# Kernel tuning notes

Hardware: AMD Instinct MI355X
Metric: run time of the kernel (lower is better)

## Reference

```python
import jax, jax.numpy as jnp
import numpy as np

N, E, F_NODE, F_EDGE, H, EH, G = 20000, 200000, 32, 8, 256, 16, 512
OUT_DIMS = [H, H, H // 2]  # 256, 256, 128
BN_EPS = 1e-5


def _lin(k, out_c, in_c):
    kw, kb = jax.random.split(k)
    bound = 1.0 / np.sqrt(in_c)
    w = jax.random.uniform(kw, (out_c, in_c), minval=-bound, maxval=bound, dtype=jnp.float32)
    b = jax.random.uniform(kb, (out_c,), minval=-bound, maxval=bound, dtype=jnp.float32)
    return w, b


def setup_inputs() -> dict:
    key = jax.random.key(0)
    ks = jax.random.split(key, 40)
    inp = {
        "x": jax.random.normal(ks[0], (N, F_NODE), dtype=jnp.float32),
        "edge_index": jax.random.randint(ks[1], (2, E), 0, N, dtype=jnp.int64),
        "edge_attr": jax.random.normal(ks[2], (E, F_EDGE), dtype=jnp.float32),
        "batch": jnp.sort(jax.random.randint(ks[3], (N,), 0, G, dtype=jnp.int64)),
    }
    inp["ee_w"], inp["ee_b"] = _lin(ks[4], EH, F_EDGE)
    inp["ne_w"], inp["ne_b"] = _lin(ks[5], H, F_NODE)
    in_dim = H
    for i, out_dim in enumerate(OUT_DIMS):
        msg_in = 2 * in_dim + EH
        inp[f"c{i}_w1"], inp[f"c{i}_b1"] = _lin(ks[6 + 2 * i], 2 * out_dim, msg_in)
        inp[f"c{i}_w2"], inp[f"c{i}_b2"] = _lin(ks[7 + 2 * i], out_dim, 2 * out_dim)
        inp[f"bn{i}_g"] = jnp.ones((out_dim,), jnp.float32)
        inp[f"bn{i}_b"] = jnp.zeros((out_dim,), jnp.float32)
        inp[f"bn{i}_m"] = jnp.zeros((out_dim,), jnp.float32)
        inp[f"bn{i}_v"] = jnp.ones((out_dim,), jnp.float32)
        in_dim = out_dim
    inp["fc_w"], inp["fc_b"] = _lin(ks[20], 12, H // 2)
    return inp


def _seg_mean(vals, idx, num):
    s = jax.ops.segment_sum(vals, idx, num_segments=num)
    cnt = jax.ops.segment_sum(jnp.ones((vals.shape[0],), vals.dtype), idx, num_segments=num)
    return s / jnp.maximum(cnt, 1.0)[:, None]


def reference(x, edge_index, edge_attr, batch,
              ee_w, ee_b, ne_w, ne_b,
              c0_w1, c0_b1, c0_w2, c0_b2,
              c1_w1, c1_b1, c1_w2, c1_b2,
              c2_w1, c2_b1, c2_w2, c2_b2,
              bn0_g, bn0_b, bn0_m, bn0_v,
              bn1_g, bn1_b, bn1_m, bn1_v,
              bn2_g, bn2_b, bn2_m, bn2_v,
              fc_w, fc_b):
    src, dst = edge_index[0], edge_index[1]  # x_j = source, x_i = target
    e = jax.nn.relu(edge_attr @ ee_w.T + ee_b)  # [E, EH]
    h = jax.nn.relu(x @ ne_w.T + ne_b)          # [N, H]
    convs = [(c0_w1, c0_b1, c0_w2, c0_b2), (c1_w1, c1_b1, c1_w2, c1_b2), (c2_w1, c2_b1, c2_w2, c2_b2)]
    bns = [(bn0_g, bn0_b, bn0_m, bn0_v), (bn1_g, bn1_b, bn1_m, bn1_v), (bn2_g, bn2_b, bn2_m, bn2_v)]
    for (w1, b1, w2, b2), (g, bb, rm, rv) in zip(convs, bns):
        m = jnp.concatenate([h[dst], h[src], e], axis=1)      # [E, 2*in + EH]
        m = jax.nn.relu(m @ w1.T + b1) @ w2.T + b2            # per-edge MLP
        h = _seg_mean(m, dst, N)                              # scatter-mean to targets
        h = jax.nn.relu((h - rm) / jnp.sqrt(rv + BN_EPS) * g + bb)  # eval-mode BN
        # dropout is identity in eval mode
    pooled = _seg_mean(h, batch, G)                           # global_mean_pool [G, H//2]
    return jax.nn.sigmoid(pooled @ fc_w.T + fc_b)             # [G, 12]
```

## Files before the change

kernel.cpp:

```cpp
#include <hip/hip_runtime.h>
#include <hip/hip_bf16.h>

typedef unsigned int  uint;
typedef unsigned short ushort;
typedef float  f32x2  __attribute__((ext_vector_type(2)));
typedef float  f32x4  __attribute__((ext_vector_type(4)));
typedef __bf16 bf16x8 __attribute__((ext_vector_type(8)));

#define DEV static __device__ __forceinline__

DEV float  b2f(ushort b){ return __uint_as_float(((uint)b) << 16); }
DEV float  lo2f(uint u){ return __uint_as_float(u << 16); }
DEV float  hi2f(uint u){ return __uint_as_float(u & 0xffff0000u); }
DEV ushort f2b(float f){
  uint u = __float_as_uint(f);
  u += 0x7fffu + ((u >> 16) & 1u);
  return (ushort)(u >> 16);
}
DEV uint pk2(float a, float b){ return (uint)f2b(a) | ((uint)f2b(b) << 16); }
DEV void unpack8(uint4 v, float* f){
  f[0]=lo2f(v.x); f[1]=hi2f(v.x); f[2]=lo2f(v.y); f[3]=hi2f(v.y);
  f[4]=lo2f(v.z); f[5]=hi2f(v.z); f[6]=lo2f(v.w); f[7]=hi2f(v.w);
}
DEV int ld_idx(const void* p, int flag, long long i){
  return flag ? ((const int*)p)[i] : (int)((const long long*)p)[i];
}
DEV int clampi(int v, int lo, int hi){ return v < lo ? lo : (v > hi ? hi : v); }

DEV void ld16(const ushort* g, ushort* l){
  __builtin_amdgcn_global_load_lds(
      (const __attribute__((address_space(1))) void*)g,
      (__attribute__((address_space(3))) void*)l, 16, 0, 0);
}

__global__ void k_probes(const uint* __restrict__ ei, const uint* __restrict__ xw,
                         int* __restrict__ iflag, int* __restrict__ fflag){
  __shared__ int anyI, cntF;
  if (threadIdx.x == 0){ anyI = 0; cntF = 0; }
  __syncthreads();
  int li = 0, lc = 0;
  for (int i = threadIdx.x; i < 1024; i += 256){
    if (ei[2*i + 1] != 0u) li = 1;
    float f = fabsf(__uint_as_float(xw[i]));
    if (f > 1e-6f && f < 1e6f) lc++;
  }
  if (li) atomicOr(&anyI, 1);
  atomicAdd(&cntF, lc);
  __syncthreads();
  if (threadIdx.x == 0){ *iflag = anyI; *fflag = (2*cntF > 1024) ? 1 : 0; }
}

__global__ __launch_bounds__(256) void k_canon(const void* __restrict__ src,
    const int* __restrict__ flag, int* __restrict__ out, int n){
  int i = blockIdx.x*256 + threadIdx.x;
  if (i >= n) return;
  out[i] = ld_idx(src, *flag, i);
}

struct CvtTab { const void* src[8]; ushort* dst[8]; int n[8]; int bstart[8]; int nseg; };
__global__ __launch_bounds__(256) void k_cvt_batch(CvtTab tab, const int* __restrict__ flag){
  int b = blockIdx.x;
  int s = tab.nseg - 1;
  for (int i = 1; i < tab.nseg; i++) if (b < tab.bstart[i]){ s = i - 1; break; }
  int rel = b - tab.bstart[s];
  const void* sp = tab.src[s];
  ushort* d = tab.dst[s];
  int f = *flag;
  int end = tab.n[s]; int cap = rel*8192 + 8192; if (cap < end) end = cap;
  for (int i = rel*8192 + threadIdx.x; i < end; i += 256)
    d[i] = f ? f2b(((const float*)sp)[i]) : ((const ushort*)sp)[i];
}

struct SmallTab { const void* src[24]; int doff[24]; int n[24]; };
__global__ __launch_bounds__(256) void k_cvt_small(SmallTab tab, const int* __restrict__ flag,
    ushort* __restrict__ base, int cnt){
  int b = blockIdx.x;
  if (b >= cnt) return;
  int f = *flag;
  const void* s = tab.src[b];
  ushort* d = base + tab.doff[b];
  for (int i = threadIdx.x; i < tab.n[b]; i += 256)
    d[i] = f ? f2b(((const float*)s)[i]) : ((const ushort*)s)[i];
}

__global__ __launch_bounds__(256) void k_count(const void* __restrict__ ei,
    const int* __restrict__ flag, int* __restrict__ cnt, int E, int N){
  int e = blockIdx.x*256 + threadIdx.x;
  if (e >= E) return;
  int d = clampi(ld_idx(ei, *flag, (long long)E + e), 0, N-1);
  atomicAdd(&cnt[d], 1);
}

__global__ __launch_bounds__(1024) void k_scan(const int* __restrict__ deg, int* __restrict__ rp, int n){
  __shared__ int part[1024];
  int t = threadIdx.x;
  int chunk = (n + 1023) >> 10;
  int base = t * chunk;
  int s = 0;
  for (int i = 0; i < chunk; i++){ int j = base + i; if (j < n) s += deg[j]; }
  part[t] = s;
  __syncthreads();
  for (int off = 1; off < 1024; off <<= 1){
    int v = (t >= off) ? part[t - off] : 0;
    __syncthreads();
    part[t] += v;
    __syncthreads();
  }
  int run = part[t] - s;
  for (int i = 0; i < chunk; i++){ int j = base + i; if (j < n){ rp[j] = run; run += deg[j]; } }
  if (t == 1023) rp[n] = part[1023];
}

__global__ __launch_bounds__(256) void k_fill(const void* __restrict__ ei,
    const int* __restrict__ flag, const int* __restrict__ rp, int* __restrict__ fill,
    int2* __restrict__ cpair, int E, int N){
  int e = blockIdx.x*256 + threadIdx.x;
  if (e >= E) return;
  int f = *flag;
  int s = clampi(ld_idx(ei, f, e), 0, N-1);
  int d = clampi(ld_idx(ei, f, (long long)E + e), 0, N-1);
  int pos = clampi(rp[d] + atomicAdd(&fill[d], 1), 0, E-1);
  cpair[pos] = make_int2(s, e);
}

__global__ __launch_bounds__(256) void k_edge_enc(const void* __restrict__ ea,
    const ushort* __restrict__ w, const ushort* __restrict__ b,
    const int* __restrict__ fflag, float* __restrict__ eh, int E){
  __shared__ float ws[128];
  __shared__ float bs[16];
  int t = threadIdx.x;
  if (t < 128) ws[t] = b2f(w[t]);
  if (t < 16)  bs[t] = b2f(b[t]);
  int f = *fflag;
  __syncthreads();
  int e = blockIdx.x*256 + t;
  if (e >= E) return;
  float a[8];
  if (f){
    const float4* ap = (const float4*)((const float*)ea + (size_t)e*8);
    float4 v0 = ap[0], v1 = ap[1];
    a[0]=v0.x; a[1]=v0.y; a[2]=v0.z; a[3]=v0.w;
    a[4]=v1.x; a[5]=v1.y; a[6]=v1.z; a[7]=v1.w;
  } else {
    uint4 av = *(const uint4*)((const ushort*)ea + (size_t)e*8);
    unpack8(av, a);
  }
  float o[16];
  #pragma unroll
  for (int c = 0; c < 16; c++){
    float s = bs[c];
    #pragma unroll
    for (int j = 0; j < 8; j++) s += a[j]*ws[c*8+j];
    o[c] = fmaxf(s, 0.f);
  }
  f32x4* op = (f32x4*)(eh + (size_t)e*16);
  #pragma unroll
  for (int q4 = 0; q4 < 4; q4++){
    f32x4 v = {o[q4*4+0], o[q4*4+1], o[q4*4+2], o[q4*4+3]};
    op[q4] = v;
  }
}

__global__ __launch_bounds__(256) void k_node_enc(const void* __restrict__ x,
    const ushort* __restrict__ w, const ushort* __restrict__ b,
    const int* __restrict__ fflag, ushort* __restrict__ h, int N){
  __shared__ float xs[4][32];
  int nb = blockIdx.x*4, t = threadIdx.x;
  int f = *fflag;
  if (t < 128){
    int ni = t >> 5, ci = t & 31;
    int n = nb + ni; if (n >= N) n = N - 1;
    xs[ni][ci] = f ? ((const float*)x)[(size_t)n*32 + ci]
                   : b2f(((const ushort*)x)[(size_t)n*32 + ci]);
  }
  __syncthreads();
  const uint4* wp = (const uint4*)(w + (size_t)t*32);
  float wr[32];
  unpack8(wp[0], wr); unpack8(wp[1], wr+8); unpack8(wp[2], wr+16); unpack8(wp[3], wr+24);
  float bv = b2f(b[t]);
  #pragma unroll
  for (int ni = 0; ni < 4; ni++){
    int n = nb + ni;
    if (n >= N) break;
    float s = bv;
    #pragma unroll
    for (int k = 0; k < 32; k++) s += xs[ni][k]*wr[k];
    h[(size_t)n*256 + t] = f2b(fmaxf(s, 0.f));
  }
}

__global__ __launch_bounds__(256) void k_gemm_pq_lds(const ushort* __restrict__ A,
    const ushort* __restrict__ w1, int M, int Nc,
    ushort* __restrict__ P, ushort* __restrict__ Q){
  __shared__ ushort As[128*32];
  __shared__ ushort Bs[128*32];
  const int t = threadIdx.x;
  const int lane = t & 63;
  const int wv = t >> 6;
  const int m0 = blockIdx.x*128;
  const int yc = Nc >> 7;
  const int isQ = (int)blockIdx.y >= yc;
  const int n0 = (isQ ? blockIdx.y - yc : blockIdx.y)*128;
  const ushort* W = w1 + (isQ ? 256 : 0);
  ushort* C = isQ ? Q : P;
  const int lr = lane & 15;
  const int qq = lane >> 4;
  int srow0 = t >> 2,         sq0 = t & 3;
  int srow1 = (256 + t) >> 2, sq1 = t & 3;
  int ga0 = m0 + srow0; if (ga0 >= M) ga0 = M - 1;
  int ga1 = m0 + srow1; if (ga1 >= M) ga1 = M - 1;
  f32x4 acc[2][8];
  #pragma unroll
  for (int f = 0; f < 2; f++)
    #pragma unroll
    for (int j = 0; j < 8; j++) acc[f][j] = {0.f,0.f,0.f,0.f};
  for (int k0 = 0; k0 < 256; k0 += 32){
    ld16(A + (size_t)ga0*256 + k0 + sq0*8, &As[(size_t)t*8]);
    ld16(A + (size_t)ga1*256 + k0 + sq1*8, &As[(size_t)(256+t)*8]);
    ld16(W + (size_t)(n0 + srow0)*528 + k0 + sq0*8, &Bs[(size_t)t*8]);
    ld16(W + (size_t)(n0 + srow1)*528 + k0 + sq1*8, &Bs[(size_t)(256+t)*8]);
    __syncthreads();
    bf16x8 a0 = *(const bf16x8*)&As[(wv*32 + lr)*32 + qq*8];
    bf16x8 a1 = *(const bf16x8*)&As[(wv*32 + 16 + lr)*32 + qq*8];
    #pragma unroll
    for (int j = 0; j < 8; j++){
      bf16x8 b = *(const bf16x8*)&Bs[(j*16 + lr)*32 + qq*8];
      acc[0][j] = __builtin_amdgcn_mfma_f32_16x16x32_bf16(a0, b, acc[0][j], 0, 0, 0);
      acc[1][j] = __builtin_amdgcn_mfma_f32_16x16x32_bf16(a1, b, acc[1][j], 0, 0, 0);
    }
    __syncthreads();
  }
  #pragma unroll
  for (int f = 0; f < 2; f++){
    #pragma unroll
    for (int r = 0; r < 4; r++){
      int row = m0 + wv*32 + f*16 + qq*4 + r;
      if (row >= M) continue;
      #pragma unroll
      for (int j = 0; j < 8; j++)
        C[(size_t)row*Nc + n0 + j*16 + lr] = f2b(acc[f][j][r]);
    }
  }
}

__global__ __launch_bounds__(256) void k_gemm_bn64(const ushort* __restrict__ A, int lda,
    const ushort* __restrict__ W, int ldb, int M, int Nc, int K,
    const ushort* __restrict__ bias, const ushort* __restrict__ g, const ushort* __restrict__ bb,
    const ushort* __restrict__ rm, const ushort* __restrict__ rv,
    const int* __restrict__ rp, ushort* __restrict__ H){
  __shared__ ushort As[64*32];
  __shared__ ushort Bs[128*32];
  const int t = threadIdx.x;
  const int lane = t & 63;
  const int wv = t >> 6;
  const int m0 = blockIdx.x*64;
  const int n0 = blockIdx.y*128;
  const int lr = lane & 15;
  const int qq = lane >> 4;
  int srowA = t >> 2, sqA = t & 3;
  int ga = m0 + srowA; if (ga >= M) ga = M - 1;
  int srowB0 = t >> 2,        srowB1 = 64 + (t >> 2);
  f32x4 acc[8];
  #pragma unroll
  for (int j = 0; j < 8; j++) acc[j] = {0.f,0.f,0.f,0.f};
  for (int k0 = 0; k0 < K; k0 += 32){
    ld16(A + (size_t)ga*lda + k0 + sqA*8, &As[(size_t)t*8]);
    ld16(W + (size_t)(n0 + srowB0)*ldb + k0 + sqA*8, &Bs[(size_t)t*8]);
    ld16(W + (size_t)(n0 + srowB1)*ldb + k0 + sqA*8, &Bs[(size_t)(256+t)*8]);
    __syncthreads();
    bf16x8 a = *(const bf16x8*)&As[(wv*16 + lr)*32 + qq*8];
    #pragma unroll
    for (int j = 0; j < 8; j++){
      bf16x8 b = *(const bf16x8*)&Bs[(j*16 + lr)*32 + qq*8];
      acc[j] = __builtin_amdgcn_mfma_f32_16x16x32_bf16(a, b, acc[j], 0, 0, 0);
    }
    __syncthreads();
  }
  float bi[8], sc[8], sh[8];
  #pragma unroll
  for (int j = 0; j < 8; j++){
    int col = n0 + j*16 + lr;
    bi[j] = b2f(bias[col]);
    sc[j] = b2f(g[col]) * rsqrtf(b2f(rv[col]) + 1e-5f);
    sh[j] = b2f(bb[col]) - b2f(rm[col]) * sc[j];
  }
  #pragma unroll
  for (int r = 0; r < 4; r++){
    int row = m0 + wv*16 + qq*4 + r;
    if (row >= M) continue;
    int empty = (rp[row+1] - rp[row] == 0);
    #pragma unroll
    for (int j = 0; j < 8; j++){
      float v = acc[j][r] + bi[j];
      if (empty) v = 0.f;
      H[(size_t)row*Nc + n0 + j*16 + lr] = f2b(fmaxf(v*sc[j] + sh[j], 0.f));
    }
  }
}

template<int C>
__global__ __launch_bounds__(256) void k_msg4(const ushort* P, const ushort* __restrict__ Q,
    const float* __restrict__ eh, const ushort* __restrict__ w1, const ushort* __restrict__ b1,
    const int* __restrict__ rp, const int2* __restrict__ cpair,
    ushort* MU, int N){
  int t = threadIdx.x;
  int c0 = t*2;
  f32x2 wc[16];
  {
    float a0[16], a1[16];
    const uint4* wp0 = (const uint4*)(w1 + (size_t)c0*528 + 512);
    const uint4* wp1 = (const uint4*)(w1 + (size_t)(c0+1)*528 + 512);
    unpack8(wp0[0], a0); unpack8(wp0[1], a0+8);
    unpack8(wp1[0], a1); unpack8(wp1[1], a1+8);
    #pragma unroll
    for (int j = 0; j < 16; j++){ wc[j].x = a0[j]; wc[j].y = a1[j]; }
  }
  uint bw = *(const uint*)(b1 + c0);
  f32x2 b1v = { lo2f(bw), hi2f(bw) };
  int nb = blockIdx.x*2;
  int ne = nb + 2; if (ne > N) ne = N;
  for (int n = nb; n < ne; n++){
    const int i0 = rp[n], i1 = rp[n+1];
    uint pw = *(const uint*)(P + (size_t)n*C + c0);
    f32x2 pre = { lo2f(pw) + b1v.x, hi2f(pw) + b1v.y };
    f32x2 acc0 = {0.f, 0.f}, acc1 = {0.f, 0.f};
    int i = i0;
    for (; i + 2 <= i1; i += 2){
      int2 p0 = cpair[i];
      int2 p1 = cpair[i+1];
      uint qw0 = *(const uint*)(Q + (size_t)p0.x*C + c0);
      uint qw1 = *(const uint*)(Q + (size_t)p1.x*C + c0);
      const f32x4* e0p = (const f32x4*)(eh + (size_t)p0.y*16);
      const f32x4* e1p = (const f32x4*)(eh + (size_t)p1.y*16);
      f32x4 ea0 = e0p[0], ea1 = e0p[1], ea2 = e0p[2], ea3 = e0p[3];
      f32x4 eb0 = e1p[0], eb1 = e1p[1], eb2 = e1p[2], eb3 = e1p[3];
      float ef0[16] = {ea0.x,ea0.y,ea0.z,ea0.w, ea1.x,ea1.y,ea1.z,ea1.w,
                       ea2.x,ea2.y,ea2.z,ea2.w, ea3.x,ea3.y,ea3.z,ea3.w};
      float ef1[16] = {eb0.x,eb0.y,eb0.z,eb0.w, eb1.x,eb1.y,eb1.z,eb1.w,
                       eb2.x,eb2.y,eb2.z,eb2.w, eb3.x,eb3.y,eb3.z,eb3.w};
      f32x2 d0 = { pre.x + lo2f(qw0), pre.y + hi2f(qw0) };
      f32x2 d1 = { pre.x + lo2f(qw1), pre.y + hi2f(qw1) };
      #pragma unroll
      for (int j = 0; j < 16; j++){
        f32x2 e0v = {ef0[j], ef0[j]};
        f32x2 e1v = {ef1[j], ef1[j]};
        d0 += wc[j] * e0v;
        d1 += wc[j] * e1v;
      }
      acc0.x += fmaxf(d0.x, 0.f); acc0.y += fmaxf(d0.y, 0.f);
      acc1.x += fmaxf(d1.x, 0.f); acc1.y += fmaxf(d1.y, 0.f);
    }
    if (i < i1){
      int2 p0 = cpair[i];
      uint qw0 = *(const uint*)(Q + (size_t)p0.x*C + c0);
      const f32x4* e0p = (const f32x4*)(eh + (size_t)p0.y*16);
      f32x4 ea0 = e0p[0], ea1 = e0p[1], ea2 = e0p[2], ea3 = e0p[3];
      float ef0[16] = {ea0.x,ea0.y,ea0.z,ea0.w, ea1.x,ea1.y,ea1.z,ea1.w,
                       ea2.x,ea2.y,ea2.z,ea2.w, ea3.x,ea3.y,ea3.z,ea3.w};
      f32x2 d0 = { pre.x + lo2f(qw0), pre.y + hi2f(qw0) };
      #pragma unroll
      for (int j = 0; j < 16; j++){
        f32x2 e0v = {ef0[j], ef0[j]};
        d0 += wc[j] * e0v;
      }
      acc0.x += fmaxf(d0.x, 0.f); acc0.y += fmaxf(d0.y, 0.f);
    }
    int cnt = i1 - i0;
    float inv = (cnt > 0) ? 1.f/(float)cnt : 0.f;
    *(uint*)(MU + (size_t)n*C + c0) = pk2((acc0.x + acc1.x)*inv, (acc0.y + acc1.y)*inv);
  }
}

__global__ __launch_bounds__(128) void k_pool(const ushort* __restrict__ h, const int* __restrict__ batch,
    const ushort* __restrict__ fw, const ushort* __restrict__ fb,
    const int* __restrict__ fflag, void* __restrict__ out, int N){
  int g = blockIdx.x, t = threadIdx.x;
  int lo = 0, hi = N;
  while (lo < hi){ int mid = (lo+hi) >> 1; if (batch[mid] <  g) lo = mid+1; else hi = mid; }
  int s0 = lo;
  hi = N;
  while (lo < hi){ int mid = (lo+hi) >> 1; if (batch[mid] <= g) lo = mid+1; else hi = mid; }
  int s1 = lo;
  float s = 0.f;
  for (int i = s0; i < s1; i++) s += b2f(h[(size_t)i*128 + t]);
  int cnt = s1 - s0;
  __shared__ float ps[128];
  ps[t] = s / (float)(cnt > 0 ? cnt : 1);
  __syncthreads();
  if (t < 12){
    float z = b2f(fb[t]);
    for (int j = 0; j < 128; j++) z += ps[j]*b2f(fw[t*128 + j]);
    float r = 1.f/(1.f + expf(-z));
    if (*fflag) ((float*)out)[g*12 + t] = r;
    else        ((ushort*)out)[g*12 + t] = f2b(r);
  }
}

__global__ __launch_bounds__(256) void k_sentinel(ushort* __restrict__ out, int n){
  int i = blockIdx.x*256 + threadIdx.x;
  if (i < n) out[i] = 0x3F00;
}

extern "C" void kernel_launch(void* const* d_in, const int* in_sizes, int n_in,
                              void* d_out, int out_size, void* d_ws, size_t ws_size,
                              hipStream_t stream){
  const void* x_raw   = d_in[0];
  const void* ei_raw  = d_in[1];
  const void* ea_raw  = d_in[2];
  const void* ba_raw  = d_in[3];
  (void)n_in;

  const int N = in_sizes[3];
  const int E = in_sizes[1] / 2;
  const int G = out_size / 12;

  char* base = (char*)d_ws;
  size_t off = 0;
  auto alloc = [&](size_t bytes)->char*{
    char* p = base + off;
    off = (off + bytes + 255) & ~(size_t)255;
    return p;
  };
  int* iflag    = (int*)alloc(256);
  int* fflag    = (int*)alloc(256);
  int* deg      = (int*)alloc((size_t)N*4);
  int* fill     = (int*)alloc((size_t)N*4);
  size_t memset_bytes = (size_t)((char*)fill - (char*)deg) + (size_t)N*4;
  int* rp       = (int*)alloc((size_t)(N+1)*4);
  int* batch2   = (int*)alloc((size_t)N*4);
  int2* cpair   = (int2*)alloc((size_t)E*8);
  ushort* new_c = (ushort*)alloc(8192*2);
  ushort* w1c[3], *w2c[3];
  const int w1n[3] = {512*528, 512*528, 256*528};
  const int w2n[3] = {256*512, 256*512, 128*256};
  for (int i = 0; i < 3; i++) w1c[i] = (ushort*)alloc((size_t)w1n[i]*2);
  for (int i = 0; i < 3; i++) w2c[i] = (ushort*)alloc((size_t)w2n[i]*2);
  ushort* smallp = (ushort*)alloc(8192*2);
  float*  e_h32 = (float*)alloc((size_t)E*16*4);
  ushort* h     = (ushort*)alloc((size_t)N*256*2);
  ushort* Q     = (ushort*)alloc((size_t)N*512*2);
  ushort* PM    = (ushort*)alloc((size_t)N*512*2);

  if (off > ws_size){
    k_sentinel<<<(out_size + 255)/256, 256, 0, stream>>>((ushort*)d_out, out_size);
    return;
  }

  k_probes<<<1, 256, 0, stream>>>((const uint*)ei_raw, (const uint*)x_raw, iflag, fflag);
  k_canon<<<(N + 255)/256, 256, 0, stream>>>(ba_raw, iflag, batch2, N);
  hipMemsetAsync(deg, 0, memset_bytes, stream);
  k_count<<<(E + 255)/256, 256, 0, stream>>>(ei_raw, iflag, deg, E, N);
  k_scan<<<1, 1024, 0, stream>>>(deg, rp, N);
  k_fill<<<(E + 255)/256, 256, 0, stream>>>(ei_raw, iflag, rp, fill, cpair, E, N);

  CvtTab ct; ct.nseg = 7;
  const void* csrcs[7] = {d_in[8], d_in[16], d_in[24], d_in[10], d_in[18], d_in[26], d_in[6]};
  ushort* cdsts[7]     = {w1c[0],  w1c[1],   w1c[2],   w2c[0],   w2c[1],   w2c[2],   new_c};
  const int cns[7]     = {w1n[0],  w1n[1],   w1n[2],   w2n[0],   w2n[1],   w2n[2],   8192};
  int bacc = 0;
  for (int i = 0; i < 7; i++){
    ct.src[i] = csrcs[i]; ct.dst[i] = cdsts[i]; ct.n[i] = cns[i];
    ct.bstart[i] = bacc; bacc += (cns[i] + 8191)/8192;
  }
  k_cvt_batch<<<bacc, 256, 0, stream>>>(ct, fflag);

  SmallTab tab;
  int scount = 0, spos = 0;
  auto addsmall = [&](int di, int n)->int{
    int p = spos;
    tab.src[scount] = d_in[di]; tab.doff[scount] = spos; tab.n[scount] = n;
    spos += n; scount++;
    return p;
  };
  int pos_eew  = addsmall(4, 128);
  int pos_eeb  = addsmall(5, 16);
  int pos_neb  = addsmall(7, 256);
  int pos_b1[3], pos_b2[3], pos_g[3], pos_bb[3], pos_m[3], pos_v[3];
  const int b1n[3] = {512,512,256}, b2n[3] = {256,256,128}, bnn[3] = {256,256,128};
  for (int i = 0; i < 3; i++){
    int di = 8 + 8*i;
    pos_b1[i] = addsmall(di+1, b1n[i]);
    pos_b2[i] = addsmall(di+3, b2n[i]);
    pos_g[i]  = addsmall(di+4, bnn[i]);
    pos_bb[i] = addsmall(di+5, bnn[i]);
    pos_m[i]  = addsmall(di+6, bnn[i]);
    pos_v[i]  = addsmall(di+7, bnn[i]);
  }
  int pos_fcw = addsmall(32, 12*128);
  int pos_fcb = addsmall(33, 12);
  k_cvt_small<<<scount, 256, 0, stream>>>(tab, fflag, smallp, scount);

  k_edge_enc<<<(E + 255)/256, 256, 0, stream>>>(ea_raw, smallp + pos_eew, smallp + pos_eeb, fflag, e_h32, E);
  k_node_enc<<<(N + 3)/4, 256, 0, stream>>>(x_raw, new_c, smallp + pos_neb, fflag, h, N);

  const int Cch[3] = {512, 512, 256};
  const int Od[3]  = {256, 256, 128};
  for (int i = 0; i < 3; i++){
    dim3 g1((N + 127)/128, 2*(Cch[i]/128));
    k_gemm_pq_lds<<<g1, 256, 0, stream>>>(h, w1c[i], N, Cch[i], PM, Q);
    dim3 gm((N + 1)/2);
    if (i < 2) k_msg4<512><<<gm, 256, 0, stream>>>(PM, Q, e_h32, w1c[i], smallp + pos_b1[i], rp, cpair, PM, N);
    else       k_msg4<256><<<gm, 128, 0, stream>>>(PM, Q, e_h32, w1c[i], smallp + pos_b1[i], rp, cpair, PM, N);
    dim3 g2((N + 63)/64, Od[i]/128 > 0 ? Od[i]/128 : 1);
    k_gemm_bn64<<<g2, 256, 0, stream>>>(PM, Cch[i], w2c[i], Cch[i], N, Od[i], Cch[i],
                                        smallp + pos_b2[i], smallp + pos_g[i], smallp + pos_bb[i],
                                        smallp + pos_m[i],  smallp + pos_v[i], rp, h);
  }

  k_pool<<<G, 128, 0, stream>>>(h, batch2, smallp + pos_fcw, smallp + pos_fcb, fflag, d_out, N);
}
```

Before: 516.2 us.

## Merge preprocessing kernels into one mega-kernel and read small params directly

Folds the flag probe and the zeroing of counters into one kernel, replacing the memset. The CSR fill, weight conversion, edge encoder and node encoder are merged into a single block-partitioned launch. The small-parameter conversion and batch canonicalisation kernels are dropped; biases, BN params, the pool weights and the batch index are now read from the raw inputs with a runtime dtype flag. This cuts launch count and serial dependencies at the cost of per-element branching on the flag.

```diff
diff --git a/kernel.cpp b/kernel.cpp
--- a/kernel.cpp
+++ b/kernel.cpp
@@ -25,6 +25,9 @@
 DEV int ld_idx(const void* p, int flag, long long i){
   return flag ? ((const int*)p)[i] : (int)((const long long*)p)[i];
 }
+DEV float ldf(const void* p, int f, int i){
+  return f ? ((const float*)p)[i] : b2f(((const ushort*)p)[i]);
+}
 DEV int clampi(int v, int lo, int hi){ return v < lo ? lo : (v > hi ? hi : v); }
 
 DEV void ld16(const ushort* g, ushort* l){
@@ -33,54 +36,26 @@
       (__attribute__((address_space(3))) void*)l, 16, 0, 0);
 }
 
-__global__ void k_probes(const uint* __restrict__ ei, const uint* __restrict__ xw,
-                         int* __restrict__ iflag, int* __restrict__ fflag){
-  __shared__ int anyI, cntF;
-  if (threadIdx.x == 0){ anyI = 0; cntF = 0; }
-  __syncthreads();
-  int li = 0, lc = 0;
-  for (int i = threadIdx.x; i < 1024; i += 256){
-    if (ei[2*i + 1] != 0u) li = 1;
-    float f = fabsf(__uint_as_float(xw[i]));
-    if (f > 1e-6f && f < 1e6f) lc++;
-  }
-  if (li) atomicOr(&anyI, 1);
-  atomicAdd(&cntF, lc);
-  __syncthreads();
-  if (threadIdx.x == 0){ *iflag = anyI; *fflag = (2*cntF > 1024) ? 1 : 0; }
-}
-
-__global__ __launch_bounds__(256) void k_canon(const void* __restrict__ src,
-    const int* __restrict__ flag, int* __restrict__ out, int n){
+__global__ __launch_bounds__(256) void k_zero_probe(const uint* __restrict__ ei,
+    const uint* __restrict__ xw, int* __restrict__ iflag, int* __restrict__ fflag,
+    int* __restrict__ zbase, int zn){
   int i = blockIdx.x*256 + threadIdx.x;
-  if (i >= n) return;
-  out[i] = ld_idx(src, *flag, i);
-}
-
-struct CvtTab { const void* src[8]; ushort* dst[8]; int n[8]; int bstart[8]; int nseg; };
-__global__ __launch_bounds__(256) void k_cvt_batch(CvtTab tab, const int* __restrict__ flag){
-  int b = blockIdx.x;
-  int s = tab.nseg - 1;
-  for (int i = 1; i < tab.nseg; i++) if (b < tab.bstart[i]){ s = i - 1; break; }
-  int rel = b - tab.bstart[s];
-  const void* sp = tab.src[s];
-  ushort* d = tab.dst[s];
-  int f = *flag;
-  int end = tab.n[s]; int cap = rel*8192 + 8192; if (cap < end) end = cap;
-  for (int i = rel*8192 + threadIdx.x; i < end; i += 256)
-    d[i] = f ? f2b(((const float*)sp)[i]) : ((const ushort*)sp)[i];
-}
-
-struct SmallTab { const void* src[24]; int doff[24]; int n[24]; };
-__global__ __launch_bounds__(256) void k_cvt_small(SmallTab tab, const int* __restrict__ flag,
-    ushort* __restrict__ base, int cnt){
-  int b = blockIdx.x;
-  if (b >= cnt) return;
-  int f = *flag;
-  const void* s = tab.src[b];
-  ushort* d = base + tab.doff[b];
-  for (int i = threadIdx.x; i < tab.n[b]; i += 256)
-    d[i] = f ? f2b(((const float*)s)[i]) : ((const ushort*)s)[i];
+  if (i < zn) zbase[i] = 0;
+  if (blockIdx.x == 0){
+    __shared__ int anyI, cntF;
+    if (threadIdx.x == 0){ anyI = 0; cntF = 0; }
+    __syncthreads();
+    int li = 0, lc = 0;
+    for (int k = threadIdx.x; k < 1024; k += 256){
+      if (ei[2*k + 1] != 0u) li = 1;
+      float f = fabsf(__uint_as_float(xw[k]));
+      if (f > 1e-6f && f < 1e6f) lc++;
+    }
+    if (li) atomicOr(&anyI, 1);
+    atomicAdd(&cntF, lc);
+    __syncthreads();
+    if (threadIdx.x == 0){ *iflag = anyI; *fflag = (2*cntF > 1024) ? 1 : 0; }
+  }
 }
 
 __global__ __launch_bounds__(256) void k_count(const void* __restrict__ ei,
@@ -111,81 +86,103 @@
   if (t == 1023) rp[n] = part[1023];
 }
 
-__global__ __launch_bounds__(256) void k_fill(const void* __restrict__ ei,
-    const int* __restrict__ flag, const int* __restrict__ rp, int* __restrict__ fill,
-    int2* __restrict__ cpair, int E, int N){
-  int e = blockIdx.x*256 + threadIdx.x;
-  if (e >= E) return;
-  int f = *flag;
-  int s = clampi(ld_idx(ei, f, e), 0, N-1);
-  int d = clampi(ld_idx(ei, f, (long long)E + e), 0, N-1);
-  int pos = clampi(rp[d] + atomicAdd(&fill[d], 1), 0, E-1);
-  cpair[pos] = make_int2(s, e);
-}
-
-__global__ __launch_bounds__(256) void k_edge_enc(const void* __restrict__ ea,
-    const ushort* __restrict__ w, const ushort* __restrict__ b,
-    const int* __restrict__ fflag, float* __restrict__ eh, int E){
-  __shared__ float ws[128];
-  __shared__ float bs[16];
+struct CvtTab { const void* src[6]; ushort* dst[6]; int n[6]; int bstart[6]; int nseg; };
+
+__global__ __launch_bounds__(256) void k_mega(
+    const void* __restrict__ ei, const int* __restrict__ iflag,
+    const int* __restrict__ rp, int* __restrict__ fill, int2* __restrict__ cpair,
+    CvtTab ct, const int* __restrict__ fflag,
+    const void* __restrict__ ea, const void* __restrict__ eew, const void* __restrict__ eeb,
+    const void* __restrict__ x, const void* __restrict__ nw, const void* __restrict__ nbias,
+    float* __restrict__ eh, ushort* __restrict__ h,
+    int E, int N, int FB, int CB, int EB){
+  int b = blockIdx.x;
   int t = threadIdx.x;
-  if (t < 128) ws[t] = b2f(w[t]);
-  if (t < 16)  bs[t] = b2f(b[t]);
-  int f = *fflag;
-  __syncthreads();
-  int e = blockIdx.x*256 + t;
-  if (e >= E) return;
-  float a[8];
-  if (f){
-    const float4* ap = (const float4*)((const float*)ea + (size_t)e*8);
-    float4 v0 = ap[0], v1 = ap[1];
-    a[0]=v0.x; a[1]=v0.y; a[2]=v0.z; a[3]=v0.w;
-    a[4]=v1.x; a[5]=v1.y; a[6]=v1.z; a[7]=v1.w;
+  if (b < FB){
+    int e = b*256 + t;
+    if (e >= E) return;
+    int f = *iflag;
+    int s = clampi(ld_idx(ei, f, e), 0, N-1);
+    int d = clampi(ld_idx(ei, f, (long long)E + e), 0, N-1);
+    int pos = clampi(rp[d] + atomicAdd(&fill[d], 1), 0, E-1);
+    cpair[pos] = make_int2(s, e);
+  } else if (b < FB + CB){
+    int cb = b - FB;
+    int s = ct.nseg - 1;
+    for (int i = 1; i < ct.nseg; i++) if (cb < ct.bstart[i]){ s = i - 1; break; }
+    int rel = cb - ct.bstart[s];
+    const void* sp = ct.src[s];
+    ushort* d = ct.dst[s];
+    int f = *fflag;
+    int end = ct.n[s]; int cap = rel*8192 + 8192; if (cap < end) end = cap;
+    for (int i = rel*8192 + t; i < end; i += 256)
+      d[i] = f ? f2b(((const float*)sp)[i]) : ((const ushort*)sp)[i];
+  } else if (b < FB + CB + EB){
+    __shared__ float ws[128];
+    __shared__ float bs[16];
+    int f = *fflag;
+    if (t < 128) ws[t] = ldf(eew, f, t);
+    if (t < 16)  bs[t] = ldf(eeb, f, t);
+    __syncthreads();
+    int e = (b - FB - CB)*256 + t;
+    if (e >= E) return;
+    float a[8];
+    if (f){
+      const float4* ap = (const float4*)((const float*)ea + (size_t)e*8);
+      float4 v0 = ap[0], v1 = ap[1];
+      a[0]=v0.x; a[1]=v0.y; a[2]=v0.z; a[3]=v0.w;
+      a[4]=v1.x; a[5]=v1.y; a[6]=v1.z; a[7]=v1.w;
+    } else {
+      uint4 av = *(const uint4*)((const ushort*)ea + (size_t)e*8);
+      unpack8(av, a);
+    }
+    float o[16];
+    #pragma unroll
+    for (int c = 0; c < 16; c++){
+      float s = bs[c];
+      #pragma unroll
+      for (int j = 0; j < 8; j++) s += a[j]*ws[c*8+j];
+      o[c] = fmaxf(s, 0.f);
+    }
+    f32x4* op = (f32x4*)(eh + (size_t)e*16);
+    #pragma unroll
+    for (int q4 = 0; q4 < 4; q4++){
+      f32x4 v = {o[q4*4+0], o[q4*4+1], o[q4*4+2], o[q4*4+3]};
+      op[q4] = v;
+    }
   } else {
-    uint4 av = *(const uint4*)((const ushort*)ea + (size_t)e*8);
-    unpack8(av, a);
-  }
-  float o[16];
-  #pragma unroll
-  for (int c = 0; c < 16; c++){
-    float s = bs[c];
-    #pragma unroll
-    for (int j = 0; j < 8; j++) s += a[j]*ws[c*8+j];
-    o[c] = fmaxf(s, 0.f);
-  }
-  f32x4* op = (f32x4*)(eh + (size_t)e*16);
-  #pragma unroll
-  for (int q4 = 0; q4 < 4; q4++){
-    f32x4 v = {o[q4*4+0], o[q4*4+1], o[q4*4+2], o[q4*4+3]};
-    op[q4] = v;
-  }
-}
-
-__global__ __launch_bounds__(256) void k_node_enc(const void* __restrict__ x,
-    const ushort* __restrict__ w, const ushort* __restrict__ b,
-    const int* __restrict__ fflag, ushort* __restrict__ h, int N){
-  __shared__ float xs[4][32];
-  int nb = blockIdx.x*4, t = threadIdx.x;
-  int f = *fflag;
-  if (t < 128){
-    int ni = t >> 5, ci = t & 31;
-    int n = nb + ni; if (n >= N) n = N - 1;
-    xs[ni][ci] = f ? ((const float*)x)[(size_t)n*32 + ci]
-                   : b2f(((const ushort*)x)[(size_t)n*32 + ci]);
-  }
-  __syncthreads();
-  const uint4* wp = (const uint4*)(w + (size_t)t*32);
-  float wr[32];
-  unpack8(wp[0], wr); unpack8(wp[1], wr+8); unpack8(wp[2], wr+16); unpack8(wp[3], wr+24);
-  float bv = b2f(b[t]);
-  #pragma unroll
-  for (int ni = 0; ni < 4; ni++){
-    int n = nb + ni;
-    if (n >= N) break;
-    float s = bv;
-    #pragma unroll
-    for (int k = 0; k < 32; k++) s += xs[ni][k]*wr[k];
-    h[(size_t)n*256 + t] = f2b(fmaxf(s, 0.f));
+    __shared__ float xs[4][32];
+    int f = *fflag;
+    int nb = (b - FB - CB - EB)*4;
+    if (t < 128){
+      int ni = t >> 5, ci = t & 31;
+      int n = nb + ni; if (n >= N) n = N - 1;
+      xs[ni][ci] = f ? ((const float*)x)[(size_t)n*32 + ci]
+                     : b2f(((const ushort*)x)[(size_t)n*32 + ci]);
+    }
+    __syncthreads();
+    float wr[32];
+    if (f){
+      const float4* wp = (const float4*)((const float*)nw + (size_t)t*32);
+      #pragma unroll
+      for (int q4 = 0; q4 < 8; q4++){
+        float4 v = wp[q4];
+        wr[q4*4+0]=v.x; wr[q4*4+1]=v.y; wr[q4*4+2]=v.z; wr[q4*4+3]=v.w;
+      }
+    } else {
+      const uint4* wp = (const uint4*)((const ushort*)nw + (size_t)t*32);
+      unpack8(wp[0], wr); unpack8(wp[1], wr+8); unpack8(wp[2], wr+16); unpack8(wp[3], wr+24);
+    }
+    float bv = ldf(nbias, f, t);
+    #pragma unroll
+    for (int ni = 0; ni < 4; ni++){
+      int n = nb + ni;
+      if (n >= N) break;
+      float s = bv;
+      #pragma unroll
+      for (int k = 0; k < 32; k++) s += xs[ni][k]*wr[k];
+      h[(size_t)n*256 + t] = f2b(fmaxf(s, 0.f));
+    }
   }
 }
 
@@ -245,8 +242,8 @@
 
 __global__ __launch_bounds__(256) void k_gemm_bn64(const ushort* __restrict__ A, int lda,
     const ushort* __restrict__ W, int ldb, int M, int Nc, int K,
-    const ushort* __restrict__ bias, const ushort* __restrict__ g, const ushort* __restrict__ bb,
-    const ushort* __restrict__ rm, const ushort* __restrict__ rv,
+    const void* __restrict__ bias, const void* __restrict__ g, const void* __restrict__ bb,
+    const void* __restrict__ rm, const void* __restrict__ rv, const int* __restrict__ fflag,
     const int* __restrict__ rp, ushort* __restrict__ H){
   __shared__ ushort As[64*32];
   __shared__ ushort Bs[128*32];
@@ -276,13 +273,14 @@
     }
     __syncthreads();
   }
+  int f = *fflag;
   float bi[8], sc[8], sh[8];
   #pragma unroll
   for (int j = 0; j < 8; j++){
     int col = n0 + j*16 + lr;
-    bi[j] = b2f(bias[col]);
-    sc[j] = b2f(g[col]) * rsqrtf(b2f(rv[col]) + 1e-5f);
-    sh[j] = b2f(bb[col]) - b2f(rm[col]) * sc[j];
+    bi[j] = ldf(bias, f, col);
+    sc[j] = ldf(g, f, col) * rsqrtf(ldf(rv, f, col) + 1e-5f);
+    sh[j] = ldf(bb, f, col) - ldf(rm, f, col) * sc[j];
   }
   #pragma unroll
   for (int r = 0; r < 4; r++){
@@ -300,8 +298,8 @@
 
 template<int C>
 __global__ __launch_bounds__(256) void k_msg4(const ushort* P, const ushort* __restrict__ Q,
-    const float* __restrict__ eh, const ushort* __restrict__ w1, const ushort* __restrict__ b1,
-    const int* __restrict__ rp, const int2* __restrict__ cpair,
+    const float* __restrict__ eh, const ushort* __restrict__ w1, const void* __restrict__ b1,
+    const int* __restrict__ fflag, const int* __restrict__ rp, const int2* __restrict__ cpair,
     ushort* MU, int N){
   int t = threadIdx.x;
   int c0 = t*2;
@@ -315,8 +313,8 @@
     #pragma unroll
     for (int j = 0; j < 16; j++){ wc[j].x = a0[j]; wc[j].y = a1[j]; }
   }
-  uint bw = *(const uint*)(b1 + c0);
-  f32x2 b1v = { lo2f(bw), hi2f(bw) };
+  int ff = *fflag;
+  f32x2 b1v = { ldf(b1, ff, c0), ldf(b1, ff, c0+1) };
   int nb = blockIdx.x*2;
   int ne = nb + 2; if (ne > N) ne = N;
   for (int n = nb; n < ne; n++){
@@ -371,15 +369,16 @@
   }
 }
 
-__global__ __launch_bounds__(128) void k_pool(const ushort* __restrict__ h, const int* __restrict__ batch,
-    const ushort* __restrict__ fw, const ushort* __restrict__ fb,
+__global__ __launch_bounds__(128) void k_pool(const ushort* __restrict__ h, const void* __restrict__ batch,
+    const int* __restrict__ iflag, const void* __restrict__ fw, const void* __restrict__ fb,
     const int* __restrict__ fflag, void* __restrict__ out, int N){
   int g = blockIdx.x, t = threadIdx.x;
+  int ifl = *iflag;
   int lo = 0, hi = N;
-  while (lo < hi){ int mid = (lo+hi) >> 1; if (batch[mid] <  g) lo = mid+1; else hi = mid; }
+  while (lo < hi){ int mid = (lo+hi) >> 1; if (ld_idx(batch, ifl, mid) <  g) lo = mid+1; else hi = mid; }
   int s0 = lo;
   hi = N;
-  while (lo < hi){ int mid = (lo+hi) >> 1; if (batch[mid] <= g) lo = mid+1; else hi = mid; }
+  while (lo < hi){ int mid = (lo+hi) >> 1; if (ld_idx(batch, ifl, mid) <= g) lo = mid+1; else hi = mid; }
   int s1 = lo;
   float s = 0.f;
   for (int i = s0; i < s1; i++) s += b2f(h[(size_t)i*128 + t]);
@@ -387,12 +386,13 @@
   __shared__ float ps[128];
   ps[t] = s / (float)(cnt > 0 ? cnt : 1);
   __syncthreads();
+  int f = *fflag;
   if (t < 12){
-    float z = b2f(fb[t]);
-    for (int j = 0; j < 128; j++) z += ps[j]*b2f(fw[t*128 + j]);
+    float z = ldf(fb, f, t);
+    for (int j = 0; j < 128; j++) z += ps[j]*ldf(fw, f, t*128 + j);
     float r = 1.f/(1.f + expf(-z));
-    if (*fflag) ((float*)out)[g*12 + t] = r;
-    else        ((ushort*)out)[g*12 + t] = f2b(r);
+    if (f) ((float*)out)[g*12 + t] = r;
+    else   ((ushort*)out)[g*12 + t] = f2b(r);
   }
 }
 
@@ -425,17 +425,14 @@
   int* fflag    = (int*)alloc(256);
   int* deg      = (int*)alloc((size_t)N*4);
   int* fill     = (int*)alloc((size_t)N*4);
-  size_t memset_bytes = (size_t)((char*)fill - (char*)deg) + (size_t)N*4;
+  int zn        = (int)(fill - deg) + N;
   int* rp       = (int*)alloc((size_t)(N+1)*4);
-  int* batch2   = (int*)alloc((size_t)N*4);
   int2* cpair   = (int2*)alloc((size_t)E*8);
-  ushort* new_c = (ushort*)alloc(8192*2);
   ushort* w1c[3], *w2c[3];
   const int w1n[3] = {512*528, 512*528, 256*528};
   const int w2n[3] = {256*512, 256*512, 128*256};
   for (int i = 0; i < 3; i++) w1c[i] = (ushort*)alloc((size_t)w1n[i]*2);
   for (int i = 0; i < 3; i++) w2c[i] = (ushort*)alloc((size_t)w2n[i]*2);
-  ushort* smallp = (ushort*)alloc(8192*2);
   float*  e_h32 = (float*)alloc((size_t)E*16*4);
   ushort* h     = (ushort*)alloc((size_t)N*256*2);
   ushort* Q     = (ushort*)alloc((size_t)N*512*2);
@@ -446,66 +443,43 @@
     return;
   }
 
-  k_probes<<<1, 256, 0, stream>>>((const uint*)ei_raw, (const uint*)x_raw, iflag, fflag);
-  k_canon<<<(N + 255)/256, 256, 0, stream>>>(ba_raw, iflag, batch2, N);
-  hipMemsetAsync(deg, 0, memset_bytes, stream);
+  k_zero_probe<<<(zn + 255)/256, 256, 0, stream>>>((const uint*)ei_raw, (const uint*)x_raw,
+                                                   iflag, fflag, deg, zn);
   k_count<<<(E + 255)/256, 256, 0, stream>>>(ei_raw, iflag, deg, E, N);
   k_scan<<<1, 1024, 0, stream>>>(deg, rp, N);
-  k_fill<<<(E + 255)/256, 256, 0, stream>>>(ei_raw, iflag, rp, fill, cpair, E, N);
-
-  CvtTab ct; ct.nseg = 7;
-  const void* csrcs[7] = {d_in[8], d_in[16], d_in[24], d_in[10], d_in[18], d_in[26], d_in[6]};
-  ushort* cdsts[7]     = {w1c[0],  w1c[1],   w1c[2],   w2c[0],   w2c[1],   w2c[2],   new_c};
-  const int cns[7]     = {w1n[0],  w1n[1],   w1n[2],   w2n[0],   w2n[1],   w2n[2],   8192};
+
+  CvtTab ct; ct.nseg = 6;
+  const void* csrcs[6] = {d_in[8], d_in[16], d_in[24], d_in[10], d_in[18], d_in[26]};
+  ushort* cdsts[6]     = {w1c[0],  w1c[1],   w1c[2],   w2c[0],   w2c[1],   w2c[2]};
+  const int cns[6]     = {w1n[0],  w1n[1],   w1n[2],   w2n[0],   w2n[1],   w2n[2]};
   int bacc = 0;
-  for (int i = 0; i < 7; i++){
+  for (int i = 0; i < 6; i++){
     ct.src[i] = csrcs[i]; ct.dst[i] = cdsts[i]; ct.n[i] = cns[i];
     ct.bstart[i] = bacc; bacc += (cns[i] + 8191)/8192;
   }
-  k_cvt_batch<<<bacc, 256, 0, stream>>>(ct, fflag);
-
-  SmallTab tab;
-  int scount = 0, spos = 0;
-  auto addsmall = [&](int di, int n)->int{
-    int p = spos;
-    tab.src[scount] = d_in[di]; tab.doff[scount] = spos; tab.n[scount] = n;
-    spos += n; scount++;
-    return p;
-  };
-  int pos_eew  = addsmall(4, 128);
-  int pos_eeb  = addsmall(5, 16);
-  int pos_neb  = addsmall(7, 256);
-  int pos_b1[3], pos_b2[3], pos_g[3], pos_bb[3], pos_m[3], pos_v[3];
-  const int b1n[3] = {512,512,256}, b2n[3] = {256,256,128}, bnn[3] = {256,256,128};
-  for (int i = 0; i < 3; i++){
-    int di = 8 + 8*i;
-    pos_b1[i] = addsmall(di+1, b1n[i]);
-    pos_b2[i] = addsmall(di+3, b2n[i]);
-    pos_g[i]  = addsmall(di+4, bnn[i]);
-    pos_bb[i] = addsmall(di+5, bnn[i]);
-    pos_m[i]  = addsmall(di+6, bnn[i]);
-    pos_v[i]  = addsmall(di+7, bnn[i]);
-  }
-  int pos_fcw = addsmall(32, 12*128);
-  int pos_fcb = addsmall(33, 12);
-  k_cvt_small<<<scount, 256, 0, stream>>>(tab, fflag, smallp, scount);
-
-  k_edge_enc<<<(E + 255)/256, 256, 0, stream>>>(ea_raw, smallp + pos_eew, smallp + pos_eeb, fflag, e_h32, E);
-  k_node_enc<<<(N + 3)/4, 256, 0, stream>>>(x_raw, new_c, smallp + pos_neb, fflag, h, N);
+  int FB = (E + 255)/256;
+  int CB = bacc;
+  int EB = (E + 255)/256;
+  int NB = (N + 3)/4;
+  k_mega<<<FB + CB + EB + NB, 256, 0, stream>>>(
+      ei_raw, iflag, rp, fill, cpair, ct, fflag,
+      ea_raw, d_in[4], d_in[5], x_raw, d_in[6], d_in[7],
+      e_h32, h, E, N, FB, CB, EB);
 
   const int Cch[3] = {512, 512, 256};
   const int Od[3]  = {256, 256, 128};
   for (int i = 0; i < 3; i++){
+    int di = 8 + 8*i;
     dim3 g1((N + 127)/128, 2*(Cch[i]/128));
     k_gemm_pq_lds<<<g1, 256, 0, stream>>>(h, w1c[i], N, Cch[i], PM, Q);
     dim3 gm((N + 1)/2);
-    if (i < 2) k_msg4<512><<<gm, 256, 0, stream>>>(PM, Q, e_h32, w1c[i], smallp + pos_b1[i], rp, cpair, PM, N);
-    else       k_msg4<256><<<gm, 128, 0, stream>>>(PM, Q, e_h32, w1c[i], smallp + pos_b1[i], rp, cpair, PM, N);
+    if (i < 2) k_msg4<512><<<gm, 256, 0, stream>>>(PM, Q, e_h32, w1c[i], d_in[di+1], fflag, rp, cpair, PM, N);
+    else       k_msg4<256><<<gm, 128, 0, stream>>>(PM, Q, e_h32, w1c[i], d_in[di+1], fflag, rp, cpair, PM, N);
     dim3 g2((N + 63)/64, Od[i]/128 > 0 ? Od[i]/128 : 1);
     k_gemm_bn64<<<g2, 256, 0, stream>>>(PM, Cch[i], w2c[i], Cch[i], N, Od[i], Cch[i],
-                                        smallp + pos_b2[i], smallp + pos_g[i], smallp + pos_bb[i],
-                                        smallp + pos_m[i],  smallp + pos_v[i], rp, h);
-  }
-
-  k_pool<<<G, 128, 0, stream>>>(h, batch2, smallp + pos_fcw, smallp + pos_fcb, fflag, d_out, N);
-}
+                                        d_in[di+3], d_in[di+4], d_in[di+5],
+                                        d_in[di+6], d_in[di+7], fflag, rp, h);
+  }
+
+  k_pool<<<G, 128, 0, stream>>>(h, ba_raw, iflag, d_in[32], d_in[33], fflag, d_out, N);
+}
```

Result: faster. 502.2 us, median of 2 (-2.7%).
